# Optimization experiments

Hardware: AMD Instinct MI355X
Metric: run time of the kernel (lower is better)

Reference implementation:

```python
import jax, jax.numpy as jnp
import numpy as np

B, TE, T = 256, 300, 600
NIN, NPV, H, EMB, NS, NHE = 128, 5, 512, 32, 4, 16
SCALE = 1.0 / float(np.sqrt(H))


def gru_cell(h, x, Wih, Whh, bih, bhh):
    # PyTorch GRU cell: r,z,n gate ordering
    gi = x @ Wih.T + bih
    gh = h @ Whh.T + bhh
    i_r, i_z, i_n = jnp.split(gi, 3, axis=-1)
    h_r, h_z, h_n = jnp.split(gh, 3, axis=-1)
    r = jax.nn.sigmoid(i_r + h_r)
    z = jax.nn.sigmoid(i_z + h_z)
    n = jnp.tanh(i_n + r * h_n)
    return (1.0 - z) * n + z * h


def setup_inputs():
    key = jax.random.key(0)
    ks = iter(jax.random.split(key, 40))
    w = lambda shape: jax.random.normal(next(ks), shape, jnp.float32) * SCALE
    inp = {
        'x_cv': jax.random.normal(next(ks), (B, TE, NIN), jnp.float32),
        'x_cv_target': jax.random.normal(next(ks), (B, T, NIN), jnp.float32),
        'pv_init': jax.random.normal(next(ks), (B, NPV), jnp.float32),
        'scenario': jax.random.randint(next(ks), (B,), 0, NS),
        'emb': w((NS, EMB)),
        'enc_Wih0': w((3 * H, NIN + EMB)), 'enc_Whh0': w((3 * H, H)), 'enc_bih0': w((3 * H,)), 'enc_bhh0': w((3 * H,)),
        'enc_Wih1': w((3 * H, H)), 'enc_Whh1': w((3 * H, H)), 'enc_bih1': w((3 * H,)), 'enc_bhh1': w((3 * H,)),
        'dec_Wih0': w((3 * H, NIN + NPV)), 'dec_Whh0': w((3 * H, H)), 'dec_bih0': w((3 * H,)), 'dec_bhh0': w((3 * H,)),
        'dec_Wih1': w((3 * H, H)), 'dec_Whh1': w((3 * H, H)), 'dec_bih1': w((3 * H,)), 'dec_bhh1': w((3 * H,)),
        'fc1_W': w((128, H)), 'fc1_b': w((128,)), 'fc2_W': w((NPV, 128)), 'fc2_b': w((NPV,)),
        'he1_W': w((128, H)), 'he1_b': w((128,)), 'he2_W': w((NHE, 128)), 'he2_b': w((NHE,)),
    }
    return inp


def _forward(x_cv, x_cv_target, pv_init, scenario, emb, enc_Wih0, enc_Whh0, enc_bih0, enc_bhh0, enc_Wih1, enc_Whh1, enc_bih1, enc_bhh1, dec_Wih0, dec_Whh0, dec_bih0, dec_bhh0, dec_Wih1, dec_Whh1, dec_bih1, dec_bhh1, fc1_W, fc1_b, fc2_W, fc2_b, he1_W, he1_b, he2_W, he2_b):
    Bb = x_cv.shape[0]
    Hh = enc_Whh0.shape[1]
    emb_s = emb[scenario]  # (B, EMB)
    enc_in = jnp.concatenate([x_cv, jnp.broadcast_to(emb_s[:, None, :], (Bb, x_cv.shape[1], emb.shape[1]))], axis=-1)
    x_t = jnp.swapaxes(enc_in, 0, 1)  # (TE, B, NIN+EMB)
    h0 = jnp.zeros((Bb, Hh), enc_in.dtype)

    def step0(h, xt):
        hn = gru_cell(h, xt, enc_Wih0, enc_Whh0, enc_bih0, enc_bhh0)
        return hn, hn
    h1_fin, seq1 = jax.lax.scan(step0, h0, x_t)

    def step1(h, xt):
        hn = gru_cell(h, xt, enc_Wih1, enc_Whh1, enc_bih1, enc_bhh1)
        return hn, hn
    h2_fin, _ = jax.lax.scan(step1, h0, seq1)

    xt_tgt = jnp.swapaxes(x_cv_target, 0, 1)  # (T, B, NIN)

    def dec_step(carry, xt):
        d1, d2, pv = carry
        inp = jnp.concatenate([xt, pv], axis=-1)
        d1 = gru_cell(d1, inp, dec_Wih0, dec_Whh0, dec_bih0, dec_bhh0)
        d2 = gru_cell(d2, d1, dec_Wih1, dec_Whh1, dec_bih1, dec_bhh1)
        pv_new = jnp.maximum(d2 @ fc1_W.T + fc1_b, 0.0) @ fc2_W.T + fc2_b
        he_new = jnp.maximum(d2 @ he1_W.T + he1_b, 0.0) @ he2_W.T + he2_b
        return (d1, d2, pv_new), (pv_new, he_new)

    _, (pv_seq, he_seq) = jax.lax.scan(dec_step, (h1_fin, h2_fin, pv_init), xt_tgt)
    pv_out = jnp.swapaxes(pv_seq, 0, 1)  # (B, T, NPV)
    he_out = jnp.swapaxes(he_seq, 0, 1)  # (B, T, NHE)
    return pv_out, he_out


def reference(x_cv, x_cv_target, pv_init, scenario, emb, enc_Wih0, enc_Whh0, enc_bih0, enc_bhh0, enc_Wih1, enc_Whh1, enc_bih1, enc_bhh1, dec_Wih0, dec_Whh0, dec_bih0, dec_bhh0, dec_Wih1, dec_Whh1, dec_bih1, dec_bhh1, fc1_W, fc1_b, fc2_W, fc2_b, he1_W, he1_b, he2_W, he2_b):
    return _forward(x_cv, x_cv_target, pv_init, scenario, emb, enc_Wih0, enc_Whh0, enc_bih0, enc_bhh0, enc_Wih1, enc_Whh1, enc_bih1, enc_bhh1, dec_Wih0, dec_Whh0, dec_bih0, dec_bhh0, dec_Wih1, dec_Whh1, dec_bih1, dec_bhh1, fc1_W, fc1_b, fc2_W, fc2_b, he1_W, he1_b, he2_W, he2_b)
```

## Files before the change

### kernel.cpp

```cpp
#include <hip/hip_runtime.h>

#define NTHR 512
#define NBLK 256

#define B_    256
#define TE_   300
#define T_    600
#define NIN_  128
#define H_    512
#define EMB_  32
#define KE0_  160
#define KD0_  136
#define OUT_HE_OFS 768000ull

#define ACT_F (32 * 68)
#define W_F   (48 * 68)

constexpr size_t OF_BAR  = 0;
constexpr size_t OF_XEMB = 1024;
constexpr size_t OF_HA   = OF_XEMB + 8192;
constexpr size_t OF_HB   = OF_HA + 262144;
constexpr size_t OF_PV   = OF_HB + 262144;
constexpr size_t OF_S1   = OF_PV + 2048;
constexpr size_t OF_S2   = OF_S1 + 32768;
constexpr size_t OF_E0I  = OF_S2 + 32768;
constexpr size_t OF_E0H  = OF_E0I + 245760;
constexpr size_t OF_E1I  = OF_E0H + 786432;
constexpr size_t OF_E1H  = OF_E1I + 786432;
constexpr size_t OF_D0I  = OF_E1H + 786432;
constexpr size_t OF_D0H  = OF_D0I + 208896;
constexpr size_t OF_D1I  = OF_D0H + 786432;
constexpr size_t OF_D1H  = OF_D1I + 786432;
constexpr size_t OF_FH   = OF_D1H + 786432;
constexpr size_t WS_END  = OF_FH + 131072;

__global__ void k_init(float* __restrict__ ws, const float* __restrict__ pv_init,
                       const int* __restrict__ scen, const float* __restrict__ emb) {
  const size_t total = 1024 + 8192 + 2048 + 131072 + 131072;
  size_t stride = (size_t)gridDim.x * blockDim.x;
  for (size_t x = (size_t)blockIdx.x * blockDim.x + threadIdx.x; x < total; x += stride) {
    if (x < 1024) {
      ((unsigned*)ws)[x] = 0u;
    } else if (x < 1024 + 8192) {
      size_t r = x - 1024; int b = (int)(r >> 5), e = (int)(r & 31);
      ws[OF_XEMB + r] = emb[scen[b] * EMB_ + e];
    } else if (x < 1024 + 8192 + 2048) {
      size_t r = x - 1024 - 8192; int b = (int)(r >> 3), p = (int)(r & 7);
      ws[OF_PV + r] = (p < 5) ? pv_init[b * 5 + p] : 0.f;
    } else if (x < 1024 + 8192 + 2048 + 131072) {
      ws[OF_HA + 131072 + (x - 1024 - 8192 - 2048)] = 0.f;
    } else {
      ws[OF_HB + 131072 + (x - 1024 - 8192 - 2048 - 131072)] = 0.f;
    }
  }
}

__global__ void k_rearr(float* __restrict__ dst, const float* __restrict__ src, int K, int Kp) {
  int n = 32 * 48 * Kp;
  for (int idx = blockIdx.x * blockDim.x + threadIdx.x; idx < n; idx += gridDim.x * blockDim.x) {
    int g = idx / (48 * Kp), r = idx % (48 * Kp), c = r / Kp, k = r % Kp;
    int j = (c >> 4) * 512 + g * 16 + (c & 15);
    dst[idx] = (k < K) ? src[j * K + k] : 0.f;
  }
}
__global__ void k_rearr_fh(float* __restrict__ dst, const float* __restrict__ fc1,
                           const float* __restrict__ he1) {
  int n = 32 * 8 * 512;
  for (int idx = blockIdx.x * blockDim.x + threadIdx.x; idx < n; idx += gridDim.x * blockDim.x) {
    int g = idx / (8 * 512), r = idx % (8 * 512), c = r / 512, k = r % 512;
    const float* s = (c < 4) ? fc1 : he1;
    dst[idx] = s[(g * 4 + (c & 3)) * 512 + k];
  }
}

__device__ __forceinline__ float sigm(float x) { return 1.f / (1.f + __expf(-x)); }
__device__ __forceinline__ float tanhx(float x) { float e = __expf(2.f * x); return 1.f - 2.f / (e + 1.f); }

__device__ __forceinline__ void bar_sync_bi(unsigned* bar, int big) {
  __syncthreads();
  if (threadIdx.x == 0) {
    unsigned* cnt = &bar[big << 6];
    unsigned* gen = &bar[(big << 6) + 16];
    unsigned g0 = __hip_atomic_load(gen, __ATOMIC_RELAXED, __HIP_MEMORY_SCOPE_AGENT);
    unsigned n = __hip_atomic_fetch_add(cnt, 1u, __ATOMIC_ACQ_REL, __HIP_MEMORY_SCOPE_AGENT);
    if (n == 31u) {
      __hip_atomic_store(cnt, 0u, __ATOMIC_RELAXED, __HIP_MEMORY_SCOPE_AGENT);
      __hip_atomic_store(gen, g0 + 1u, __ATOMIC_RELEASE, __HIP_MEMORY_SCOPE_AGENT);
    } else {
      while (__hip_atomic_load(gen, __ATOMIC_ACQUIRE, __HIP_MEMORY_SCOPE_AGENT) == g0)
        __builtin_amdgcn_s_sleep(1);
    }
  }
  __syncthreads();
}

#define GCHUNK(Q, AX0, AX1)                                                                  \
  {                                                                                          \
    const int q_ = (Q);                                                                      \
    const float4 a0 = A4c[r0 * 17 + q_];                                                     \
    const float4 a1 = A4c[r1 * 17 + q_];                                                     \
    const float4 wr = W4c[hc * 17 + q_];                                                     \
    const float4 wz = W4c[(16 + hc) * 17 + q_];                                              \
    const float4 wn = W4c[(32 + hc) * 17 + q_];                                              \
    aR0 = fmaf(a0.x, wr.x, aR0); aR0 = fmaf(a0.y, wr.y, aR0);                                \
    aR0 = fmaf(a0.z, wr.z, aR0); aR0 = fmaf(a0.w, wr.w, aR0);                                \
    aR1 = fmaf(a1.x, wr.x, aR1); aR1 = fmaf(a1.y, wr.y, aR1);                                \
    aR1 = fmaf(a1.z, wr.z, aR1); aR1 = fmaf(a1.w, wr.w, aR1);                                \
    aZ0 = fmaf(a0.x, wz.x, aZ0); aZ0 = fmaf(a0.y, wz.y, aZ0);                                \
    aZ0 = fmaf(a0.z, wz.z, aZ0); aZ0 = fmaf(a0.w, wz.w, aZ0);                                \
    aZ1 = fmaf(a1.x, wz.x, aZ1); aZ1 = fmaf(a1.y, wz.y, aZ1);                                \
    aZ1 = fmaf(a1.z, wz.z, aZ1); aZ1 = fmaf(a1.w, wz.w, aZ1);                                \
    AX0 = fmaf(a0.x, wn.x, AX0); AX0 = fmaf(a0.y, wn.y, AX0);                                \
    AX0 = fmaf(a0.z, wn.z, AX0); AX0 = fmaf(a0.w, wn.w, AX0);                                \
    AX1 = fmaf(a1.x, wn.x, AX1); AX1 = fmaf(a1.y, wn.y, AX1);                                \
    AX1 = fmaf(a1.z, wn.z, AX1); AX1 = fmaf(a1.w, wn.w, AX1);                                \
  }

template <int KIND, int KI>
__device__ __forceinline__ void stage_pref(
    int kt, int tid, int b0, int g, int t,
    const float* __restrict__ actA, const float* __restrict__ actB,
    const float* __restrict__ wi, const float* __restrict__ wh,
    const float* __restrict__ hprev,
    float4& wv0, float4& wv1, float4& av, bool& w0v, bool& w1v, bool& a_v) {
  constexpr int NTI = (KI + 63) >> 6;
  w0v = false; w1v = false; a_v = false;
  if (kt < NTI) {
    const int k0 = kt << 6;
    const int cnt = (KI - k0 >= 64) ? 64 : (KI - k0);
    const int L = (cnt == 64) ? 4 : (cnt == 32) ? 3 : 1;
    const int M = (1 << L) - 1;
    if (tid < (48 << L)) {
      w0v = true;
      const int c0 = tid >> L, f0 = tid & M;
      wv0 = *(const float4*)(wi + (size_t)(g * 48 + c0) * KI + k0 + (f0 << 2));
    }
    const int i1 = tid + 512;
    if (i1 < (48 << L)) {
      w1v = true;
      const int c1 = i1 >> L, f1 = i1 & M;
      wv1 = *(const float4*)(wi + (size_t)(g * 48 + c1) * KI + k0 + (f1 << 2));
    }
    if (tid < (32 << L)) {
      const int row = tid >> L, f = tid & M;
      if (KIND == 1) {
        av = *(const float4*)(actA + (size_t)(b0 + row) * H_ + k0 + (f << 2)); a_v = true;
      } else if (KIND == 0) {
        if (k0 < 128) {
          av = *(const float4*)(actA + ((size_t)(b0 + row) * TE_ + t) * NIN_ + k0 + (f << 2)); a_v = true;
        } else {
          av = *(const float4*)(actB + (size_t)(b0 + row) * EMB_ + (f << 2)); a_v = true;
        }
      } else {
        if (k0 < 128) {
          av = *(const float4*)(actA + ((size_t)(b0 + row) * T_ + t) * NIN_ + k0 + (f << 2)); a_v = true;
        }
      }
    }
  } else {
    const int k0 = (kt - NTI) << 6;
    w0v = true;
    wv0 = *(const float4*)(wh + (size_t)(g * 48 + (tid >> 4)) * 512 + k0 + ((tid & 15) << 2));
    if (tid < 256) {
      w1v = true;
      wv1 = *(const float4*)(wh + (size_t)(g * 48 + 32 + (tid >> 4)) * 512 + k0 + ((tid & 15) << 2));
    }
    av = *(const float4*)(hprev + (size_t)(b0 + (tid >> 4)) * H_ + k0 + ((tid & 15) << 2));
    a_v = true;
  }
}

template <int KIND, int KI>
__device__ __forceinline__ void stage_write(
    int kt, int tid, float* __restrict__ s_act_b, float* __restrict__ s_w_b,
    const float4& wv0, const float4& wv1, const float4& av,
    bool w0v, bool w1v, bool a_v, const float* __restrict__ s_pvl) {
  constexpr int NTI = (KI + 63) >> 6;
  const bool is_input = (kt < NTI);
  const int k0i = kt << 6;
  const int cnt = is_input ? ((KI - k0i >= 64) ? 64 : (KI - k0i)) : 64;
  const int L = (cnt == 64) ? 4 : (cnt == 32) ? 3 : 1;
  const int M = (1 << L) - 1;
  float4* W4 = (float4*)s_w_b;
  float4* A4 = (float4*)s_act_b;
  if (w0v) W4[(tid >> L) * 17 + (tid & M)] = wv0;
  if (w1v) { const int i1 = tid + 512; W4[(i1 >> L) * 17 + (i1 & M)] = wv1; }
  if (a_v) A4[(tid >> L) * 17 + (tid & M)] = av;
  if (KIND == 2 && is_input && k0i == 128 && tid < 64) {
    const int row = tid >> 1, f = tid & 1;
    float4 v;
    if (f == 0) {
      v.x = s_pvl[(row << 3) + 0]; v.y = s_pvl[(row << 3) + 1];
      v.z = s_pvl[(row << 3) + 2]; v.w = s_pvl[(row << 3) + 3];
    } else {
      v.x = s_pvl[(row << 3) + 4]; v.y = 0.f; v.z = 0.f; v.w = 0.f;
    }
    A4[row * 17 + f] = v;
  }
}

template <int KIND, int KI>
__device__ void gru_tile(const float* __restrict__ actA, const float* __restrict__ actB, int t,
                         const float* __restrict__ wi, const float* __restrict__ wh,
                         const float* __restrict__ bi, const float* __restrict__ bh,
                         const float* __restrict__ hprev, float* __restrict__ hout,
                         int b0, int g, float* __restrict__ s_act, float* __restrict__ s_w,
                         float* __restrict__ s_sb, const float* __restrict__ s_pvl) {
  const int tid = threadIdx.x;
  const int hc = tid & 15;
  const int rp = (tid >> 4) & 15;
  const int ks = tid >> 8;
  const int r0 = rp << 1, r1 = r0 + 1;
  float aR0 = 0.f, aR1 = 0.f, aZ0 = 0.f, aZ1 = 0.f;
  float aX0 = 0.f, aX1 = 0.f, aN0 = 0.f, aN1 = 0.f;
  constexpr int NTI = (KI + 63) >> 6;
  constexpr int NTT = NTI + 8;

  float4 wv0 = {0,0,0,0}, wv1 = {0,0,0,0}, av = {0,0,0,0};
  bool w0v = false, w1v = false, a_v = false;
  stage_pref<KIND, KI>(0, tid, b0, g, t, actA, actB, wi, wh, hprev, wv0, wv1, av, w0v, w1v, a_v);
  stage_write<KIND, KI>(0, tid, s_act, s_w, wv0, wv1, av, w0v, w1v, a_v, s_pvl);

  for (int kt = 0; kt < NTT; ++kt) {
    const bool is_input = (kt < NTI);
    const int k0i = kt << 6;
    const int cnt = is_input ? ((KI - k0i >= 64) ? 64 : (KI - k0i)) : 64;
    const int cur = kt & 1;

    __syncthreads();
    if (kt + 1 < NTT)
      stage_pref<KIND, KI>(kt + 1, tid, b0, g, t, actA, actB, wi, wh, hprev, wv0, wv1, av, w0v, w1v, a_v);

    const float4* A4c = (const float4*)(s_act + cur * ACT_F);
    const float4* W4c = (const float4*)(s_w + cur * W_F);
    if (is_input) {
      if (cnt == 64) {
        const int qb = ks << 3;
#pragma unroll 2
        for (int ch = 0; ch < 8; ++ch) GCHUNK(qb + ch, aX0, aX1)
      } else if (cnt == 32) {
        const int qb = ks << 2;
#pragma unroll 2
        for (int ch = 0; ch < 4; ++ch) GCHUNK(qb + ch, aX0, aX1)
      } else {
        GCHUNK(ks, aX0, aX1)
      }
    } else {
      const int qb = ks << 3;
#pragma unroll 2
      for (int ch = 0; ch < 8; ++ch) GCHUNK(qb + ch, aN0, aN1)
    }

    if (kt + 1 < NTT)
      stage_write<KIND, KI>(kt + 1, tid, s_act + (cur ^ 1) * ACT_F, s_w + (cur ^ 1) * W_F,
                            wv0, wv1, av, w0v, w1v, a_v, s_pvl);
  }

  if (ks) {
    float* rb = s_sb + (size_t)(tid & 255) * 9;
    rb[0] = aR0; rb[1] = aR1; rb[2] = aZ0; rb[3] = aZ1;
    rb[4] = aX0; rb[5] = aX1; rb[6] = aN0; rb[7] = aN1;
  }
  __syncthreads();
  if (!ks) {
    const float* rb = s_sb + (size_t)tid * 9;
    aR0 += rb[0]; aR1 += rb[1]; aZ0 += rb[2]; aZ1 += rb[3];
    aX0 += rb[4]; aX1 += rb[5]; aN0 += rb[6]; aN1 += rb[7];
    const int hid = (g << 4) + hc;
    const float biR = bi[hid] + bh[hid];
    const float biZ = bi[512 + hid] + bh[512 + hid];
    const float biN = bi[1024 + hid], bhN = bh[1024 + hid];
    {
      const float r = sigm(aR0 + biR), z = sigm(aZ0 + biZ);
      const float n = tanhx(aX0 + biN + r * (aN0 + bhN));
      const float hp = hprev[(size_t)(b0 + r0) * H_ + hid];
      hout[(size_t)(b0 + r0) * H_ + hid] = (1.f - z) * n + z * hp;
    }
    {
      const float r = sigm(aR1 + biR), z = sigm(aZ1 + biZ);
      const float n = tanhx(aX1 + biN + r * (aN1 + bhN));
      const float hp = hprev[(size_t)(b0 + r1) * H_ + hid];
      hout[(size_t)(b0 + r1) * H_ + hid] = (1.f - z) * n + z * hp;
    }
  }
}

__global__ __launch_bounds__(NTHR, 1) void k_main(
    float* __restrict__ ws, const float* __restrict__ x_cv, const float* __restrict__ x_tgt,
    const float* __restrict__ e_bi0, const float* __restrict__ e_bh0,
    const float* __restrict__ e_bi1, const float* __restrict__ e_bh1,
    const float* __restrict__ d_bi0, const float* __restrict__ d_bh0,
    const float* __restrict__ d_bi1, const float* __restrict__ d_bh1,
    const float* __restrict__ fc1_b, const float* __restrict__ fc2_W, const float* __restrict__ fc2_b,
    const float* __restrict__ he1_b, const float* __restrict__ he2_W, const float* __restrict__ he2_b,
    float* __restrict__ out) {
  __shared__ __align__(16) float s_act[2 * ACT_F];
  __shared__ __align__(16) float s_w[2 * W_F];
  __shared__ __align__(16) float s_pv[256];
  __shared__ __align__(16) float s_sb[32 * 132];

  const int tid = threadIdx.x;
  const int wg = blockIdx.x;
  const int ji = wg & 31;
  const int bi = wg >> 5;
  const int b0 = bi << 5;

  unsigned* bar = (unsigned*)ws;
  float* xemb = ws + OF_XEMB;
  float* hA[2] = {ws + OF_HA, ws + OF_HA + 131072};
  float* hB[2] = {ws + OF_HB, ws + OF_HB + 131072};
  float* pvst = ws + OF_PV;
  float* s1g = ws + OF_S1;
  float* s2g = ws + OF_S2;
  const float* wE0I = ws + OF_E0I; const float* wE0H = ws + OF_E0H;
  const float* wE1I = ws + OF_E1I; const float* wE1H = ws + OF_E1H;
  const float* wD0I = ws + OF_D0I; const float* wD0H = ws + OF_D0H;
  const float* wD1I = ws + OF_D1I; const float* wD1H = ws + OF_D1H;
  const float* wFH  = ws + OF_FH;

  for (int s = 0; s <= TE_; ++s) {
    if (s < TE_)
      gru_tile<0, KE0_>(x_cv, xemb, s, wE0I, wE0H, e_bi0, e_bh0,
                        hA[(s + 1) & 1], hA[s & 1], b0, ji, s_act, s_w, s_sb, nullptr);
    if (s >= 1)
      gru_tile<1, 512>(hA[(s + 1) & 1], nullptr, 0, wE1I, wE1H, e_bi1, e_bh1,
                       hB[s & 1], hB[(s + 1) & 1], b0, ji, s_act, s_w, s_sb, nullptr);
    bar_sync_bi(bar, bi);
  }

  for (int t = 0; t <= T_; ++t) {
    if (t == 0) {
      if (tid < 256) s_pv[tid] = pvst[(b0 << 3) + tid];
      __syncthreads();
    } else {
      {
        int row = tid >> 4, co = (tid & 15) << 3;
        float4 v0 = *(const float4*)(s1g + (size_t)(b0 + row) * 128 + co);
        float4 v1 = *(const float4*)(s1g + (size_t)(b0 + row) * 128 + co + 4);
        *(float4*)(s_sb + row * 132 + co) = v0;
        *(float4*)(s_sb + row * 132 + co + 4) = v1;
      }
      __syncthreads();
      if (tid < 160) {
        int bl2 = tid & 31, p = tid >> 5;
        float acc = fc2_b[p];
        const float4* sb4 = (const float4*)(s_sb + bl2 * 132);
        const float4* w4 = (const float4*)(fc2_W + p * 128);
#pragma unroll 8
        for (int c = 0; c < 32; ++c) {
          float4 a = sb4[c], w = w4[c];
          acc = fmaf(a.x, w.x, acc); acc = fmaf(a.y, w.y, acc);
          acc = fmaf(a.z, w.z, acc); acc = fmaf(a.w, w.w, acc);
        }
        s_pv[(bl2 << 3) + p] = acc;
      }
      __syncthreads();
      if (ji == 1 && tid < 160) {
        int bl2 = tid & 31, p = tid >> 5;
        out[((size_t)(b0 + bl2) * T_ + (t - 1)) * 5 + p] = s_pv[(bl2 << 3) + p];
      }
      if (ji == 0) {
        int row = tid >> 4, co = (tid & 15) << 3;
        float4 v0 = *(const float4*)(s2g + (size_t)(b0 + row) * 128 + co);
        float4 v1 = *(const float4*)(s2g + (size_t)(b0 + row) * 128 + co + 4);
        *(float4*)(s_sb + row * 132 + co) = v0;
        *(float4*)(s_sb + row * 132 + co + 4) = v1;
        __syncthreads();
        int bl2 = tid & 31, e = tid >> 5;
        float acc = he2_b[e];
        const float4* sb4 = (const float4*)(s_sb + bl2 * 132);
        const float4* w4 = (const float4*)(he2_W + e * 128);
#pragma unroll 8
        for (int c = 0; c < 32; ++c) {
          float4 a = sb4[c], w = w4[c];
          acc = fmaf(a.x, w.x, acc); acc = fmaf(a.y, w.y, acc);
          acc = fmaf(a.z, w.z, acc); acc = fmaf(a.w, w.w, acc);
        }
        out[OUT_HE_OFS + ((size_t)(b0 + bl2) * T_ + (t - 1)) * 16 + e] = acc;
      }
    }

    if (t < T_) {
      gru_tile<2, KD0_>(x_tgt, nullptr, t, wD0I, wD0H, d_bi0, d_bh0,
                        hA[(t + 1) & 1], hA[t & 1], b0, ji, s_act, s_w, s_sb, s_pv);
      bar_sync_bi(bar, bi);
      gru_tile<1, 512>(hA[t & 1], nullptr, 0, wD1I, wD1H, d_bi1, d_bh1,
                       hB[(t + 1) & 1], hB[t & 1], b0, ji, s_act, s_w, s_sb, nullptr);
      bar_sync_bi(bar, bi);
      {
        const float* d2 = hB[t & 1];
        const int c = tid & 7;
        const int rp2 = (tid >> 3) & 15;
        const int ks2 = tid >> 7;
        const int r0h = rp2 << 1, r1h = r0h + 1;
        float aF0 = 0.f, aF1 = 0.f;
        float4 wv = {0,0,0,0}, av;
        if (tid < 128)
          wv = *(const float4*)(wFH + (size_t)((ji << 3) + (tid >> 4)) * 512 + ((tid & 15) << 2));
        av = *(const float4*)(d2 + (size_t)(b0 + (tid >> 4)) * H_ + ((tid & 15) << 2));
        {
          float4* W4 = (float4*)s_w;
          float4* A4 = (float4*)s_act;
          if (tid < 128) W4[(tid >> 4) * 17 + (tid & 15)] = wv;
          A4[(tid >> 4) * 17 + (tid & 15)] = av;
        }
        for (int kt = 0; kt < 8; ++kt) {
          const int cur = kt & 1;
          __syncthreads();
          if (kt + 1 < 8) {
            const int k0 = (kt + 1) << 6;
            if (tid < 128)
              wv = *(const float4*)(wFH + (size_t)((ji << 3) + (tid >> 4)) * 512 + k0 + ((tid & 15) << 2));
            av = *(const float4*)(d2 + (size_t)(b0 + (tid >> 4)) * H_ + k0 + ((tid & 15) << 2));
          }
          const float4* A4c = (const float4*)(s_act + cur * ACT_F);
          const float4* W4c = (const float4*)(s_w + cur * W_F);
          const int qb = ks2 << 2;
#pragma unroll 2
          for (int ch = 0; ch < 4; ++ch) {
            const int q_ = qb + ch;
            const float4 a0 = A4c[r0h * 17 + q_];
            const float4 a1 = A4c[r1h * 17 + q_];
            const float4 w = W4c[c * 17 + q_];
            aF0 = fmaf(a0.x, w.x, aF0); aF0 = fmaf(a0.y, w.y, aF0);
            aF0 = fmaf(a0.z, w.z, aF0); aF0 = fmaf(a0.w, w.w, aF0);
            aF1 = fmaf(a1.x, w.x, aF1); aF1 = fmaf(a1.y, w.y, aF1);
            aF1 = fmaf(a1.z, w.z, aF1); aF1 = fmaf(a1.w, w.w, aF1);
          }
          if (kt + 1 < 8) {
            float4* W4 = (float4*)(s_w + (cur ^ 1) * W_F);
            float4* A4 = (float4*)(s_act + (cur ^ 1) * ACT_F);
            if (tid < 128) W4[(tid >> 4) * 17 + (tid & 15)] = wv;
            A4[(tid >> 4) * 17 + (tid & 15)] = av;
          }
        }
        if (ks2) {
          float* rbf = s_sb + (size_t)(tid & 127) * 9 + ((ks2 - 1) << 1);
          rbf[0] = aF0; rbf[1] = aF1;
        }
        __syncthreads();
        if (tid < 128) {
          const float* rbf = s_sb + (size_t)tid * 9;
          aF0 += rbf[0] + rbf[2] + rbf[4];
          aF1 += rbf[1] + rbf[3] + rbf[5];
          if (c < 4) {
            const float bb = fc1_b[(ji << 2) + c];
            s1g[(size_t)(b0 + r0h) * 128 + (ji << 2) + c] = fmaxf(aF0 + bb, 0.f);
            s1g[(size_t)(b0 + r1h) * 128 + (ji << 2) + c] = fmaxf(aF1 + bb, 0.f);
          } else {
            const float bb = he1_b[(ji << 2) + c - 4];
            s2g[(size_t)(b0 + r0h) * 128 + (ji << 2) + c - 4] = fmaxf(aF0 + bb, 0.f);
            s2g[(size_t)(b0 + r1h) * 128 + (ji << 2) + c - 4] = fmaxf(aF1 + bb, 0.f);
          }
        }
      }
      bar_sync_bi(bar, bi);
    }
  }
}

extern "C" void kernel_launch(void* const* d_in, const int* in_sizes, int n_in,
                              void* d_out, int out_size, void* d_ws, size_t ws_size,
                              hipStream_t stream) {
  float* ws = (float*)d_ws;
  const float* x_cv   = (const float*)d_in[0];
  const float* x_tgt  = (const float*)d_in[1];
  const float* pv_init= (const float*)d_in[2];
  const int*   scen   = (const int*)d_in[3];
  const float* emb    = (const float*)d_in[4];
  const float* eWih0  = (const float*)d_in[5];
  const float* eWhh0  = (const float*)d_in[6];
  const float* ebi0   = (const float*)d_in[7];
  const float* ebh0   = (const float*)d_in[8];
  const float* eWih1  = (const float*)d_in[9];
  const float* eWhh1  = (const float*)d_in[10];
  const float* ebi1   = (const float*)d_in[11];
  const float* ebh1   = (const float*)d_in[12];
  const float* dWih0  = (const float*)d_in[13];
  const float* dWhh0  = (const float*)d_in[14];
  const float* dbi0   = (const float*)d_in[15];
  const float* dbh0   = (const float*)d_in[16];
  const float* dWih1  = (const float*)d_in[17];
  const float* dWhh1  = (const float*)d_in[18];
  const float* dbi1   = (const float*)d_in[19];
  const float* dbh1   = (const float*)d_in[20];
  const float* fc1W   = (const float*)d_in[21];
  const float* fc1b   = (const float*)d_in[22];
  const float* fc2W   = (const float*)d_in[23];
  const float* fc2b   = (const float*)d_in[24];
  const float* he1W   = (const float*)d_in[25];
  const float* he1b   = (const float*)d_in[26];
  const float* he2W   = (const float*)d_in[27];
  const float* he2b   = (const float*)d_in[28];

  hipLaunchKernelGGL(k_init, dim3(512), dim3(256), 0, stream, ws, pv_init, scen, emb);
  hipLaunchKernelGGL(k_rearr, dim3(512), dim3(256), 0, stream, ws + OF_E0I, eWih0, 160, 160);
  hipLaunchKernelGGL(k_rearr, dim3(512), dim3(256), 0, stream, ws + OF_E0H, eWhh0, 512, 512);
  hipLaunchKernelGGL(k_rearr, dim3(512), dim3(256), 0, stream, ws + OF_E1I, eWih1, 512, 512);
  hipLaunchKernelGGL(k_rearr, dim3(512), dim3(256), 0, stream, ws + OF_E1H, eWhh1, 512, 512);
  hipLaunchKernelGGL(k_rearr, dim3(512), dim3(256), 0, stream, ws + OF_D0I, dWih0, 133, 136);
  hipLaunchKernelGGL(k_rearr, dim3(512), dim3(256), 0, stream, ws + OF_D0H, dWhh0, 512, 512);
  hipLaunchKernelGGL(k_rearr, dim3(512), dim3(256), 0, stream, ws + OF_D1I, dWih1, 512, 512);
  hipLaunchKernelGGL(k_rearr, dim3(512), dim3(256), 0, stream, ws + OF_D1H, dWhh1, 512, 512);
  hipLaunchKernelGGL(k_rearr_fh, dim3(256), dim3(256), 0, stream, ws + OF_FH, fc1W, he1W);

  hipLaunchKernelGGL(k_main, dim3(NBLK), dim3(NTHR), 0, stream,
                     ws, x_cv, x_tgt, ebi0, ebh0, ebi1, ebh1, dbi0, dbh0, dbi1, dbh1,
                     fc1b, fc2W, fc2b, he1b, he2W, he2b, (float*)d_out);
}
```

Measured before the change: 74.86 ms.

## Retile GRU gate matmul to 4 rows per thread with wave-shuffle K reduction

Changes the per-thread register tile from 2 batch rows with a 2-way K split to 4 batch rows with a 4-way K split inside a wavefront. Each weight float4 loaded from LDS is now reused across four activation rows, cutting LDS weight traffic per FMA. The partial sums are combined with cross-lane shuffles instead of a shared-memory scratch buffer, and every thread then finalizes one output element. The cost is higher register pressure (16 accumulators) and extra shuffle instructions, plus possible LDS bank conflicts from the new access pattern.

```diff
diff --git a/kernel.cpp b/kernel.cpp
--- a/kernel.cpp
+++ b/kernel.cpp
@@ -94,26 +94,22 @@
   __syncthreads();
 }
 
-#define GCHUNK(Q, AX0, AX1)                                                                  \
-  {                                                                                          \
-    const int q_ = (Q);                                                                      \
-    const float4 a0 = A4c[r0 * 17 + q_];                                                     \
-    const float4 a1 = A4c[r1 * 17 + q_];                                                     \
-    const float4 wr = W4c[hc * 17 + q_];                                                     \
-    const float4 wz = W4c[(16 + hc) * 17 + q_];                                              \
-    const float4 wn = W4c[(32 + hc) * 17 + q_];                                              \
-    aR0 = fmaf(a0.x, wr.x, aR0); aR0 = fmaf(a0.y, wr.y, aR0);                                \
-    aR0 = fmaf(a0.z, wr.z, aR0); aR0 = fmaf(a0.w, wr.w, aR0);                                \
-    aR1 = fmaf(a1.x, wr.x, aR1); aR1 = fmaf(a1.y, wr.y, aR1);                                \
-    aR1 = fmaf(a1.z, wr.z, aR1); aR1 = fmaf(a1.w, wr.w, aR1);                                \
-    aZ0 = fmaf(a0.x, wz.x, aZ0); aZ0 = fmaf(a0.y, wz.y, aZ0);                                \
-    aZ0 = fmaf(a0.z, wz.z, aZ0); aZ0 = fmaf(a0.w, wz.w, aZ0);                                \
-    aZ1 = fmaf(a1.x, wz.x, aZ1); aZ1 = fmaf(a1.y, wz.y, aZ1);                                \
-    aZ1 = fmaf(a1.z, wz.z, aZ1); aZ1 = fmaf(a1.w, wz.w, aZ1);                                \
-    AX0 = fmaf(a0.x, wn.x, AX0); AX0 = fmaf(a0.y, wn.y, AX0);                                \
-    AX0 = fmaf(a0.z, wn.z, AX0); AX0 = fmaf(a0.w, wn.w, AX0);                                \
-    AX1 = fmaf(a1.x, wn.x, AX1); AX1 = fmaf(a1.y, wn.y, AX1);                                \
-    AX1 = fmaf(a1.z, wn.z, AX1); AX1 = fmaf(a1.w, wn.w, AX1);                                \
+#define FMA4(ACC, AV, WV)                                   \
+  ACC = fmaf(AV.x, WV.x, ACC); ACC = fmaf(AV.y, WV.y, ACC); \
+  ACC = fmaf(AV.z, WV.z, ACC); ACC = fmaf(AV.w, WV.w, ACC);
+
+#define GQ4(Q, AX)                                                                   \
+  { const int q_ = (Q);                                                              \
+    const float4 wr = W4c[hc * 17 + q_];                                             \
+    const float4 wz = W4c[(16 + hc) * 17 + q_];                                      \
+    const float4 wn = W4c[(32 + hc) * 17 + q_];                                      \
+    const float4 a0 = A4c[(rb + 0) * 17 + q_];                                       \
+    const float4 a1 = A4c[(rb + 1) * 17 + q_];                                       \
+    const float4 a2 = A4c[(rb + 2) * 17 + q_];                                       \
+    const float4 a3 = A4c[(rb + 3) * 17 + q_];                                       \
+    FMA4(aR[0], a0, wr) FMA4(aR[1], a1, wr) FMA4(aR[2], a2, wr) FMA4(aR[3], a3, wr)  \
+    FMA4(aZ[0], a0, wz) FMA4(aZ[1], a1, wz) FMA4(aZ[2], a2, wz) FMA4(aZ[3], a3, wz)  \
+    FMA4(AX[0], a0, wn) FMA4(AX[1], a1, wn) FMA4(AX[2], a2, wn) FMA4(AX[3], a3, wn)  \
   }
 
 template <int KIND, int KI>
@@ -208,11 +204,11 @@
                          float* __restrict__ s_sb, const float* __restrict__ s_pvl) {
   const int tid = threadIdx.x;
   const int hc = tid & 15;
-  const int rp = (tid >> 4) & 15;
-  const int ks = tid >> 8;
-  const int r0 = rp << 1, r1 = r0 + 1;
-  float aR0 = 0.f, aR1 = 0.f, aZ0 = 0.f, aZ1 = 0.f;
-  float aX0 = 0.f, aX1 = 0.f, aN0 = 0.f, aN1 = 0.f;
+  const int ks = (tid >> 4) & 3;
+  const int rq = tid >> 6;
+  const int rb = rq << 2;
+  float aR[4] = {0.f,0.f,0.f,0.f}, aZ[4] = {0.f,0.f,0.f,0.f};
+  float aX[4] = {0.f,0.f,0.f,0.f}, aN[4] = {0.f,0.f,0.f,0.f};
   constexpr int NTI = (KI + 63) >> 6;
   constexpr int NTT = NTI + 8;
 
@@ -235,20 +231,20 @@
     const float4* W4c = (const float4*)(s_w + cur * W_F);
     if (is_input) {
       if (cnt == 64) {
-        const int qb = ks << 3;
-#pragma unroll 2
-        for (int ch = 0; ch < 8; ++ch) GCHUNK(qb + ch, aX0, aX1)
-      } else if (cnt == 32) {
         const int qb = ks << 2;
 #pragma unroll 2
-        for (int ch = 0; ch < 4; ++ch) GCHUNK(qb + ch, aX0, aX1)
+        for (int ch = 0; ch < 4; ++ch) GQ4(qb + ch, aX)
+      } else if (cnt == 32) {
+        const int qb = ks << 1;
+#pragma unroll 2
+        for (int ch = 0; ch < 2; ++ch) GQ4(qb + ch, aX)
       } else {
-        GCHUNK(ks, aX0, aX1)
+        if (ks < 2) GQ4(ks, aX)
       }
     } else {
-      const int qb = ks << 3;
+      const int qb = ks << 2;
 #pragma unroll 2
-      for (int ch = 0; ch < 8; ++ch) GCHUNK(qb + ch, aN0, aN1)
+      for (int ch = 0; ch < 4; ++ch) GQ4(qb + ch, aN)
     }
 
     if (kt + 1 < NTT)
@@ -256,32 +252,28 @@
                             wv0, wv1, av, w0v, w1v, a_v, s_pvl);
   }
 
-  if (ks) {
-    float* rb = s_sb + (size_t)(tid & 255) * 9;
-    rb[0] = aR0; rb[1] = aR1; rb[2] = aZ0; rb[3] = aZ1;
-    rb[4] = aX0; rb[5] = aX1; rb[6] = aN0; rb[7] = aN1;
-  }
   __syncthreads();
-  if (!ks) {
-    const float* rb = s_sb + (size_t)tid * 9;
-    aR0 += rb[0]; aR1 += rb[1]; aZ0 += rb[2]; aZ1 += rb[3];
-    aX0 += rb[4]; aX1 += rb[5]; aN0 += rb[6]; aN1 += rb[7];
+
+#pragma unroll
+  for (int j = 0; j < 4; ++j) {
+    aR[j] += __shfl_xor(aR[j], 16); aR[j] += __shfl_xor(aR[j], 32);
+    aZ[j] += __shfl_xor(aZ[j], 16); aZ[j] += __shfl_xor(aZ[j], 32);
+    aX[j] += __shfl_xor(aX[j], 16); aX[j] += __shfl_xor(aX[j], 32);
+    aN[j] += __shfl_xor(aN[j], 16); aN[j] += __shfl_xor(aN[j], 32);
+  }
+
+  {
+    const float sR = (ks & 2) ? ((ks & 1) ? aR[3] : aR[2]) : ((ks & 1) ? aR[1] : aR[0]);
+    const float sZ = (ks & 2) ? ((ks & 1) ? aZ[3] : aZ[2]) : ((ks & 1) ? aZ[1] : aZ[0]);
+    const float sX = (ks & 2) ? ((ks & 1) ? aX[3] : aX[2]) : ((ks & 1) ? aX[1] : aX[0]);
+    const float sN = (ks & 2) ? ((ks & 1) ? aN[3] : aN[2]) : ((ks & 1) ? aN[1] : aN[0]);
     const int hid = (g << 4) + hc;
-    const float biR = bi[hid] + bh[hid];
-    const float biZ = bi[512 + hid] + bh[512 + hid];
-    const float biN = bi[1024 + hid], bhN = bh[1024 + hid];
-    {
-      const float r = sigm(aR0 + biR), z = sigm(aZ0 + biZ);
-      const float n = tanhx(aX0 + biN + r * (aN0 + bhN));
-      const float hp = hprev[(size_t)(b0 + r0) * H_ + hid];
-      hout[(size_t)(b0 + r0) * H_ + hid] = (1.f - z) * n + z * hp;
-    }
-    {
-      const float r = sigm(aR1 + biR), z = sigm(aZ1 + biZ);
-      const float n = tanhx(aX1 + biN + r * (aN1 + bhN));
-      const float hp = hprev[(size_t)(b0 + r1) * H_ + hid];
-      hout[(size_t)(b0 + r1) * H_ + hid] = (1.f - z) * n + z * hp;
-    }
+    const int row = rb + ks;
+    const float r = sigm(sR + bi[hid] + bh[hid]);
+    const float z = sigm(sZ + bi[512 + hid] + bh[512 + hid]);
+    const float n = tanhx(sX + bi[1024 + hid] + r * (sN + bh[1024 + hid]));
+    const float hp = hprev[(size_t)(b0 + row) * H_ + hid];
+    hout[(size_t)(b0 + row) * H_ + hid] = (1.f - z) * n + z * hp;
   }
 }
 
```

After: 75.92 ms. Within noise of the previous version (+1.4%).
